# Performance work log

Hardware: AMD Instinct MI355X
Metric: run time of the kernel (lower is better)

The kernel has to match this reference:

```python
import jax, jax.numpy as jnp
import numpy as np

LR = 0.1          # learning_rate
THRESHOLD = 0.1   # surprise_threshold (fixed; adaptive_threshold=False / eval path)
TEMP = 0.1        # temperature
EPS = 1e-6

B, S, DK, DV = 64, 1024, 128, 128


def setup_inputs() -> dict:
    key = jax.random.key(0)
    k1, k2 = jax.random.split(key)
    return {
        "memory": jnp.zeros((B, DV, DK), dtype=jnp.float32),
        "key": jax.random.normal(k1, (B, S, DK), dtype=jnp.float32),
        "value": jax.random.normal(k2, (B, S, DV), dtype=jnp.float32),
    }


def reference(memory, key, value):
    # memory: (B, DV, DK); key: (B, S, DK); value: (B, S, DV)
    # Sequential delta-rule fast-weight update with surprise gating.
    def step(mem, kv):
        k_t, v_t = kv                                  # (B, DK), (B, DV)
        k_n = k_t / (jnp.linalg.norm(k_t, axis=-1, keepdims=True) + EPS)
        predicted = jnp.einsum('bvk,bk->bv', mem, k_n)  # (B, DV)
        surprise = predicted - v_t                      # (B, DV)
        s_norm = jnp.linalg.norm(surprise, axis=-1, keepdims=True)  # (B, 1)
        gate = jax.nn.sigmoid((s_norm - THRESHOLD) / TEMP)          # (B, 1)
        # forget_term + lr*learn_term = (predicted + lr*surprise) outer k_n
        update = (predicted + LR * surprise)[:, :, None] * k_n[:, None, :]
        mem = mem - gate[:, :, None] * update
        return mem, gate

    # scan over the sequence axis
    kv_seq = (jnp.swapaxes(key, 0, 1), jnp.swapaxes(value, 0, 1))  # (S, B, *)
    mem_final, gates = jax.lax.scan(step, memory, kv_seq)
    gate_values = jnp.swapaxes(gates, 0, 1)  # (B, S, 1)
    return mem_final, gate_values
```

## Files before the change

### kernel.cpp

```cpp
#include <hip/hip_runtime.h>
#include <math.h>

#define B_    64
#define S_    1024
#define DK_   128
#define DV_   128
#define T_    16
#define NC_   (S_ / T_)
#define KP_   (DK_ + 4)
#define LR_   0.1f
#define LRP1_ 1.1f
#define THR_  0.1f
#define ITEMP_ 10.0f
#define EPS_  1e-6f

template<int CTRL>
__device__ __forceinline__ float dpp_add(float x) {
  int t = __builtin_amdgcn_update_dpp(0, __float_as_int(x), CTRL, 0xf, 0xf, true);
  return x + __int_as_float(t);
}
__device__ __forceinline__ float wave_sum64(float x) {
  x = dpp_add<0x111>(x); x = dpp_add<0x112>(x); x = dpp_add<0x114>(x);
  x = dpp_add<0x118>(x); x = dpp_add<0x142>(x); x = dpp_add<0x143>(x);
  return __int_as_float(__builtin_amdgcn_readlane(__float_as_int(x), 63));
}
__device__ __forceinline__ float row16_sum(float x) {
  x = dpp_add<0x111>(x); x = dpp_add<0x112>(x);
  x = dpp_add<0x114>(x); x = dpp_add<0x118>(x);
  return x;
}
__device__ __forceinline__ float rdlane(float v, int l) {
  return __int_as_float(__builtin_amdgcn_readlane(__float_as_int(v), l));
}
__device__ __forceinline__ float dot4(float4 a, float4 b) {
  return fmaf(a.x, b.x, fmaf(a.y, b.y, fmaf(a.z, b.z, a.w * b.w)));
}
__device__ __forceinline__ void gll16(const float* g, float* l) {
  __builtin_amdgcn_global_load_lds(
      (const __attribute__((address_space(1))) unsigned int*)g,
      (__attribute__((address_space(3))) unsigned int*)l, 16, 0, 0);
}

__global__ __launch_bounds__(512, 1)
void sgm_kernel(const float* __restrict__ mem_in,
                const float* __restrict__ key,
                const float* __restrict__ value,
                float* __restrict__ out) {
  const int b = blockIdx.x, tid = threadIdx.x;
  const int g = tid >> 4, h = tid & 15, lane = tid & 63, wv = tid >> 6;

  __shared__ __align__(16) float kS[4][T_][KP_];
  __shared__ __align__(16) float vS[3][T_][KP_];
  __shared__ __align__(16) float rawL[T_][DK_];
  __shared__ __align__(16) float cuL[T_][DK_];
  __shared__ __align__(16) float GT[2][T_][T_];
  __shared__ __align__(16) float gateL[S_];

  float4 mA[4], mB[4];
  {
    const float4* Mp = reinterpret_cast<const float4*>(mem_in + (size_t)b * DV_ * DK_);
    #pragma unroll
    for (int rr = 0; rr < 4; ++rr) {
      mA[rr] = Mp[(4*g + rr) * 32 + h];
      mB[rr] = Mp[(4*g + rr) * 32 + 16 + h];
    }
  }
  const float* kb = key   + (size_t)b * S_ * DK_;
  const float* vb = value + (size_t)b * S_ * DV_;

  const int pPair = (tid - 64) >> 1;
  int tP = 0, jP = 0;
  {
    int t = 0, pp = pPair;
    if (wv > 0 && pPair >= 0 && pPair < 136) {
      while (pp > t) { pp -= (t + 1); ++t; }
      tP = t; jP = pp;
    }
  }

  auto stage = [&](int cc) {
    if (wv == 0 && lane < 32) {
      #pragma unroll
      for (int t = 0; t < T_; ++t)
        gll16(kb + (size_t)(cc*T_ + t)*DK_ + lane*4, &kS[cc & 3][t][0]);
    }
    if (wv == 1 && lane < 32) {
      #pragma unroll
      for (int t = 0; t < T_; ++t)
        gll16(vb + (size_t)(cc*T_ + t)*DV_ + lane*4, &vS[cc % 3][t][0]);
    }
  };

  float4 kxR[16];

  auto applyUpdate = [&](int sl) {
    #pragma unroll
    for (int j = 0; j < T_; ++j) {
      const float4* kj = reinterpret_cast<const float4*>(&kS[sl][j][0]);
      const float4 ky = kj[16 + h];
      const float4 cu = *reinterpret_cast<const float4*>(&cuL[j][4 * g]);
      const float cc4[4] = {cu.x, cu.y, cu.z, cu.w};
      #pragma unroll
      for (int rr = 0; rr < 4; ++rr) {
        mA[rr].x = fmaf(-cc4[rr], kxR[j].x, mA[rr].x);
        mA[rr].y = fmaf(-cc4[rr], kxR[j].y, mA[rr].y);
        mA[rr].z = fmaf(-cc4[rr], kxR[j].z, mA[rr].z);
        mA[rr].w = fmaf(-cc4[rr], kxR[j].w, mA[rr].w);
        mB[rr].x = fmaf(-cc4[rr], ky.x, mB[rr].x);
        mB[rr].y = fmaf(-cc4[rr], ky.y, mB[rr].y);
        mB[rr].z = fmaf(-cc4[rr], ky.z, mB[rr].z);
        mB[rr].w = fmaf(-cc4[rr], ky.w, mB[rr].w);
      }
    }
  };

  auto gramPhase = [&](int cc) {
    const int sl = cc & 3, pb = cc & 1;
    const int h2 = tid & 1;
    if (wv > 0 && pPair < 136) {
      const float4* kj4 = reinterpret_cast<const float4*>(&kS[sl][jP][h2*64]);
      const float4* kt4 = reinterpret_cast<const float4*>(&kS[sl][tP][h2*64]);
      float acc = 0.f;
      #pragma unroll
      for (int i = 0; i < 16; ++i) {
        const int ii = (i + pPair) & 15;
        acc += dot4(kj4[ii], kt4[ii]);
      }
      int sw = __builtin_amdgcn_update_dpp(0, __float_as_int(acc), 0xB1, 0xf, 0xf, true);
      const float tot = acc + __int_as_float(sw);
      if (h2 == 0) GT[pb][tP][jP] = tot;
    }
  };

  stage(0); stage(1);
  if (wv < 2) asm volatile("s_waitcnt vmcnt(0)" ::: "memory");
  __syncthreads();
  gramPhase(0);
  asm volatile("s_waitcnt lgkmcnt(0)" ::: "memory");
  __builtin_amdgcn_s_barrier();
  asm volatile("" ::: "memory");

  for (int c = 0; c < NC_; ++c) {
    const int cb = c & 1;
    const bool staged = (c + 2 < NC_);

    if (staged) stage(c + 2);

    if (c > 0) applyUpdate((c - 1) & 3);

    #pragma unroll
    for (int t = 0; t < T_; ++t) {
      const float4* kt = reinterpret_cast<const float4*>(&kS[c & 3][t][0]);
      const float4 kx = kt[h];
      const float4 ky = kt[16 + h];
      kxR[t] = kx;
      float a0 = dot4(mA[0], kx) + dot4(mB[0], ky);
      float a1 = dot4(mA[1], kx) + dot4(mB[1], ky);
      float a2 = dot4(mA[2], kx) + dot4(mB[2], ky);
      float a3 = dot4(mA[3], kx) + dot4(mB[3], ky);
      a0 = row16_sum(a0); a1 = row16_sum(a1);
      a2 = row16_sum(a2); a3 = row16_sum(a3);
      if (h == 15)
        *reinterpret_cast<float4*>(&rawL[t][4 * g]) = make_float4(a0, a1, a2, a3);
    }

    if (wv < 2) {
      if (staged) asm volatile("s_waitcnt vmcnt(16)" ::: "memory");
      else        asm volatile("s_waitcnt vmcnt(0)"  ::: "memory");
    }
    asm volatile("s_waitcnt lgkmcnt(0)" ::: "memory");
    __builtin_amdgcn_s_barrier();
    asm volatile("" ::: "memory");

    if (wv == 0) {
      const int sj = lane & 15;
      const float rinv = 1.0f / (sqrtf(GT[cb][sj][sj]) + EPS_);
      float cu0[T_], cu1[T_];
      #pragma unroll
      for (int t = 0; t < T_; ++t) {
        const float grt = GT[cb][t][sj];
        const float rin_t = rdlane(rinv, t);
        float y0 = 0.f, y1 = 0.f;
        #pragma unroll
        for (int j = 0; j < T_; ++j) if (j < t) {
          const float gjt = rdlane(grt, j);
          y0 = fmaf(gjt, cu0[j], y0);
          y1 = fmaf(gjt, cu1[j], y1);
        }
        const float2 rv  = *reinterpret_cast<const float2*>(&rawL[t][2*lane]);
        const float2 vvt = *reinterpret_cast<const float2*>(&vS[c % 3][t][2*lane]);
        const float pred0 = rin_t * (rv.x - y0);
        const float pred1 = rin_t * (rv.y - y1);
        const float s0 = pred0 - vvt.x, s1 = pred1 - vvt.y;
        const float s2 = wave_sum64(fmaf(s0, s0, s1 * s1));
        const float gg = 1.0f / (1.0f + __expf((THR_ - sqrtf(s2)) * ITEMP_));
        if (lane == 0) gateL[c*T_ + t] = gg;
        const float ct = gg * rin_t;
        const float u0 = fmaf(LRP1_, pred0, -(LR_ * vvt.x));
        const float u1 = fmaf(LRP1_, pred1, -(LR_ * vvt.y));
        cu0[t] = ct * u0; cu1[t] = ct * u1;
        *reinterpret_cast<float2*>(&cuL[t][2*lane]) = make_float2(cu0[t], cu1[t]);
      }
    } else {
      if (c + 1 < NC_) gramPhase(c + 1);
    }

    asm volatile("s_waitcnt lgkmcnt(0)" ::: "memory");
    __builtin_amdgcn_s_barrier();
    asm volatile("" ::: "memory");
  }

  applyUpdate((NC_ - 1) & 3);

  {
    float4* Op = reinterpret_cast<float4*>(out + (size_t)b * DV_ * DK_);
    #pragma unroll
    for (int rr = 0; rr < 4; ++rr) {
      Op[(4*g + rr) * 32 + h] = mA[rr];
      Op[(4*g + rr) * 32 + 16 + h] = mB[rr];
    }
    float2* Gp = reinterpret_cast<float2*>(out + (size_t)B_ * DV_ * DK_ + (size_t)b * S_);
    Gp[tid] = reinterpret_cast<const float2*>(gateL)[tid];
  }
}

extern "C" void kernel_launch(void* const* d_in, const int* in_sizes, int n_in,
                              void* d_out, int out_size, void* d_ws, size_t ws_size,
                              hipStream_t stream) {
  const float* mem = (const float*)d_in[0];
  const float* key = (const float*)d_in[1];
  const float* val = (const float*)d_in[2];
  float* out = (float*)d_out;
  sgm_kernel<<<B_, 512, 0, stream>>>(mem, key, val, out);
}
```

Measured before the change: 543.2 us.

## Add dedicated solver wave and pipeline chunk solve behind memory matvec

Adds a ninth wavefront that runs the sequential intra-chunk triangular solve and gating for chunk c-1, while the eight memory-holding waves compute raw predictions for chunk c. This lags the memory update by two chunks and corrects the raw predictions with a cross-chunk key Gram matrix (XG). The goal is one barrier per chunk instead of two, taking the serial wave-0 solve off the critical path. In exchange it adds a 16x16 cross-Gram computation per chunk, more LDS buffering, and reloads kx from LDS instead of keeping it in registers.

Result: slower. 790.8 us (+45.6%).

```diff
diff --git a/kernel.cpp b/kernel.cpp
--- a/kernel.cpp
+++ b/kernel.cpp
@@ -41,23 +41,26 @@
       (__attribute__((address_space(3))) unsigned int*)l, 16, 0, 0);
 }
 
-__global__ __launch_bounds__(512, 1)
+__global__ __launch_bounds__(576, 1)
 void sgm_kernel(const float* __restrict__ mem_in,
                 const float* __restrict__ key,
                 const float* __restrict__ value,
                 float* __restrict__ out) {
   const int b = blockIdx.x, tid = threadIdx.x;
-  const int g = tid >> 4, h = tid & 15, lane = tid & 63, wv = tid >> 6;
-
-  __shared__ __align__(16) float kS[4][T_][KP_];
-  __shared__ __align__(16) float vS[3][T_][KP_];
-  __shared__ __align__(16) float rawL[T_][DK_];
-  __shared__ __align__(16) float cuL[T_][DK_];
+  const int wv = tid >> 6;
+  const bool mW = (wv < 8);
+  const int g = tid >> 4, h = tid & 15, lane = tid & 63;
+
+  __shared__ __align__(16) float kS[5][T_][KP_];
+  __shared__ __align__(16) float vS[4][T_][KP_];
+  __shared__ __align__(16) float rawR[2][T_][DK_];
+  __shared__ __align__(16) float cuL[2][T_][DK_];
+  __shared__ __align__(16) float XG[2][T_][T_];
   __shared__ __align__(16) float GT[2][T_][T_];
   __shared__ __align__(16) float gateL[S_];
 
   float4 mA[4], mB[4];
-  {
+  if (mW) {
     const float4* Mp = reinterpret_cast<const float4*>(mem_in + (size_t)b * DV_ * DK_);
     #pragma unroll
     for (int rr = 0; rr < 4; ++rr) {
@@ -70,42 +73,41 @@
 
   const int pPair = (tid - 64) >> 1;
   int tP = 0, jP = 0;
-  {
+  if (mW && wv > 0 && pPair < 136) {
     int t = 0, pp = pPair;
-    if (wv > 0 && pPair >= 0 && pPair < 136) {
-      while (pp > t) { pp -= (t + 1); ++t; }
-      tP = t; jP = pp;
-    }
-  }
+    while (pp > t) { pp -= (t + 1); ++t; }
+    tP = t; jP = pp;
+  }
+  const int xId = tid - 64;
+  const int xj = (xId >> 4) & 15, xt = xId & 15;
 
   auto stage = [&](int cc) {
     if (wv == 0 && lane < 32) {
       #pragma unroll
       for (int t = 0; t < T_; ++t)
-        gll16(kb + (size_t)(cc*T_ + t)*DK_ + lane*4, &kS[cc & 3][t][0]);
+        gll16(kb + (size_t)(cc*T_ + t)*DK_ + lane*4, &kS[cc % 5][t][0]);
     }
     if (wv == 1 && lane < 32) {
       #pragma unroll
       for (int t = 0; t < T_; ++t)
-        gll16(vb + (size_t)(cc*T_ + t)*DV_ + lane*4, &vS[cc % 3][t][0]);
+        gll16(vb + (size_t)(cc*T_ + t)*DV_ + lane*4, &vS[cc & 3][t][0]);
     }
   };
 
-  float4 kxR[16];
-
-  auto applyUpdate = [&](int sl) {
+  auto applyUpdate = [&](int c2) {
+    const int sl = c2 % 5;
     #pragma unroll
     for (int j = 0; j < T_; ++j) {
       const float4* kj = reinterpret_cast<const float4*>(&kS[sl][j][0]);
-      const float4 ky = kj[16 + h];
-      const float4 cu = *reinterpret_cast<const float4*>(&cuL[j][4 * g]);
+      const float4 kx = kj[h], ky = kj[16 + h];
+      const float4 cu = *reinterpret_cast<const float4*>(&cuL[c2 & 1][j][4 * g]);
       const float cc4[4] = {cu.x, cu.y, cu.z, cu.w};
       #pragma unroll
       for (int rr = 0; rr < 4; ++rr) {
-        mA[rr].x = fmaf(-cc4[rr], kxR[j].x, mA[rr].x);
-        mA[rr].y = fmaf(-cc4[rr], kxR[j].y, mA[rr].y);
-        mA[rr].z = fmaf(-cc4[rr], kxR[j].z, mA[rr].z);
-        mA[rr].w = fmaf(-cc4[rr], kxR[j].w, mA[rr].w);
+        mA[rr].x = fmaf(-cc4[rr], kx.x, mA[rr].x);
+        mA[rr].y = fmaf(-cc4[rr], kx.y, mA[rr].y);
+        mA[rr].z = fmaf(-cc4[rr], kx.z, mA[rr].z);
+        mA[rr].w = fmaf(-cc4[rr], kx.w, mA[rr].w);
         mB[rr].x = fmaf(-cc4[rr], ky.x, mB[rr].x);
         mB[rr].y = fmaf(-cc4[rr], ky.y, mB[rr].y);
         mB[rr].z = fmaf(-cc4[rr], ky.z, mB[rr].z);
@@ -114,111 +116,139 @@
     }
   };
 
-  auto gramPhase = [&](int cc) {
-    const int sl = cc & 3, pb = cc & 1;
-    const int h2 = tid & 1;
-    if (wv > 0 && pPair < 136) {
-      const float4* kj4 = reinterpret_cast<const float4*>(&kS[sl][jP][h2*64]);
-      const float4* kt4 = reinterpret_cast<const float4*>(&kS[sl][tP][h2*64]);
-      float acc = 0.f;
-      #pragma unroll
-      for (int i = 0; i < 16; ++i) {
-        const int ii = (i + pPair) & 15;
-        acc += dot4(kj4[ii], kt4[ii]);
-      }
-      int sw = __builtin_amdgcn_update_dpp(0, __float_as_int(acc), 0xB1, 0xf, 0xf, true);
-      const float tot = acc + __int_as_float(sw);
-      if (h2 == 0) GT[pb][tP][jP] = tot;
-    }
-  };
-
   stage(0); stage(1);
   if (wv < 2) asm volatile("s_waitcnt vmcnt(0)" ::: "memory");
   __syncthreads();
-  gramPhase(0);
-  asm volatile("s_waitcnt lgkmcnt(0)" ::: "memory");
-  __builtin_amdgcn_s_barrier();
-  asm volatile("" ::: "memory");
-
-  for (int c = 0; c < NC_; ++c) {
+
+  for (int c = 0; c <= NC_; ++c) {
     const int cb = c & 1;
-    const bool staged = (c + 2 < NC_);
-
-    if (staged) stage(c + 2);
-
-    if (c > 0) applyUpdate((c - 1) & 3);
-
-    #pragma unroll
-    for (int t = 0; t < T_; ++t) {
-      const float4* kt = reinterpret_cast<const float4*>(&kS[c & 3][t][0]);
-      const float4 kx = kt[h];
-      const float4 ky = kt[16 + h];
-      kxR[t] = kx;
-      float a0 = dot4(mA[0], kx) + dot4(mB[0], ky);
-      float a1 = dot4(mA[1], kx) + dot4(mB[1], ky);
-      float a2 = dot4(mA[2], kx) + dot4(mB[2], ky);
-      float a3 = dot4(mA[3], kx) + dot4(mB[3], ky);
-      a0 = row16_sum(a0); a1 = row16_sum(a1);
-      a2 = row16_sum(a2); a3 = row16_sum(a3);
-      if (h == 15)
-        *reinterpret_cast<float4*>(&rawL[t][4 * g]) = make_float4(a0, a1, a2, a3);
+
+    if (mW) {
+      if (c < NC_) {
+        if (c + 2 < NC_) stage(c + 2);
+        if (c >= 2) applyUpdate(c - 2);
+
+        const int sl = c % 5;
+        #pragma unroll
+        for (int t = 0; t < T_; ++t) {
+          const float4* kt = reinterpret_cast<const float4*>(&kS[sl][t][0]);
+          const float4 kx = kt[h], ky = kt[16 + h];
+          float a0 = dot4(mA[0], kx) + dot4(mB[0], ky);
+          float a1 = dot4(mA[1], kx) + dot4(mB[1], ky);
+          float a2 = dot4(mA[2], kx) + dot4(mB[2], ky);
+          float a3 = dot4(mA[3], kx) + dot4(mB[3], ky);
+          a0 = row16_sum(a0); a1 = row16_sum(a1);
+          a2 = row16_sum(a2); a3 = row16_sum(a3);
+          if (h == 15)
+            *reinterpret_cast<float4*>(&rawR[cb][t][4 * g]) = make_float4(a0, a1, a2, a3);
+        }
+
+        if (c >= 1 && xId >= 0 && xId < 256) {
+          const float4* a4 = reinterpret_cast<const float4*>(&kS[(c - 1) % 5][xj][0]);
+          const float4* b4 = reinterpret_cast<const float4*>(&kS[sl][xt][0]);
+          float acc = 0.f;
+          #pragma unroll
+          for (int i = 0; i < 32; ++i) {
+            const int ii = (i + xId) & 31;
+            acc += dot4(a4[ii], b4[ii]);
+          }
+          XG[cb][xj][xt] = acc;
+        }
+
+        if (wv > 0 && pPair < 136) {
+          const int h2 = tid & 1;
+          const float4* kj4 = reinterpret_cast<const float4*>(&kS[sl][jP][h2 * 64]);
+          const float4* kt4 = reinterpret_cast<const float4*>(&kS[sl][tP][h2 * 64]);
+          float acc = 0.f;
+          #pragma unroll
+          for (int i = 0; i < 16; ++i) acc += dot4(kj4[i], kt4[i]);
+          int sw = __builtin_amdgcn_update_dpp(0, __float_as_int(acc), 0xB1, 0xf, 0xf, true);
+          const float tot = acc + __int_as_float(sw);
+          if (h2 == 0) GT[cb][tP][jP] = tot;
+        }
+      } else {
+        applyUpdate(NC_ - 2);
+      }
+    } else {
+      if (c >= 1) {
+        const int sc = c - 1, sb = sc & 1;
+        const int sl16 = lane & 15;
+
+        float rv0[T_], rv1[T_];
+        #pragma unroll
+        for (int t = 0; t < T_; ++t) {
+          const float2 rr = *reinterpret_cast<const float2*>(&rawR[sb][t][2 * lane]);
+          rv0[t] = rr.x; rv1[t] = rr.y;
+        }
+        if (sc >= 1) {
+          #pragma unroll
+          for (int j = 0; j < T_; ++j) {
+            const float2 cu2 = *reinterpret_cast<const float2*>(&cuL[(sc - 1) & 1][j][2 * lane]);
+            const float4* xr = reinterpret_cast<const float4*>(&XG[sb][j][0]);
+            const float4 x0 = xr[0], x1 = xr[1], x2 = xr[2], x3 = xr[3];
+            const float xv[16] = {x0.x,x0.y,x0.z,x0.w, x1.x,x1.y,x1.z,x1.w,
+                                  x2.x,x2.y,x2.z,x2.w, x3.x,x3.y,x3.z,x3.w};
+            #pragma unroll
+            for (int t = 0; t < T_; ++t) {
+              rv0[t] = fmaf(-cu2.x, xv[t], rv0[t]);
+              rv1[t] = fmaf(-cu2.y, xv[t], rv1[t]);
+            }
+          }
+        }
+
+        float Gr[T_];
+        #pragma unroll
+        for (int t = 0; t < T_; ++t) Gr[t] = GT[sb][t][sl16];
+        const float rinv = 1.0f / (sqrtf(GT[sb][sl16][sl16]) + EPS_);
+
+        float cu0[T_], cu1[T_];
+        #pragma unroll
+        for (int t = 0; t < T_; ++t) {
+          const float rin_t = rdlane(rinv, t);
+          float y0 = 0.f, y1 = 0.f;
+          #pragma unroll
+          for (int j = 0; j < T_; ++j) if (j < t) {
+            const float gjt = rdlane(Gr[t], j);
+            y0 = fmaf(gjt, cu0[j], y0);
+            y1 = fmaf(gjt, cu1[j], y1);
+          }
+          const float2 vvt = *reinterpret_cast<const float2*>(&vS[sc & 3][t][2 * lane]);
+          const float pred0 = rin_t * (rv0[t] - y0);
+          const float pred1 = rin_t * (rv1[t] - y1);
+          const float s0 = pred0 - vvt.x, s1 = pred1 - vvt.y;
+          const float s2 = wave_sum64(fmaf(s0, s0, s1 * s1));
+          const float gg = 1.0f / (1.0f + __expf((THR_ - sqrtf(s2)) * ITEMP_));
+          if (lane == 0) gateL[sc * T_ + t] = gg;
+          const float ct = gg * rin_t;
+          const float u0 = fmaf(LRP1_, pred0, -(LR_ * vvt.x));
+          const float u1 = fmaf(LRP1_, pred1, -(LR_ * vvt.y));
+          cu0[t] = ct * u0; cu1[t] = ct * u1;
+          *reinterpret_cast<float2*>(&cuL[sb][t][2 * lane]) = make_float2(cu0[t], cu1[t]);
+        }
+      }
     }
 
     if (wv < 2) {
-      if (staged) asm volatile("s_waitcnt vmcnt(16)" ::: "memory");
-      else        asm volatile("s_waitcnt vmcnt(0)"  ::: "memory");
+      if (c + 2 < NC_) asm volatile("s_waitcnt vmcnt(16)" ::: "memory");
+      else             asm volatile("s_waitcnt vmcnt(0)"  ::: "memory");
     }
     asm volatile("s_waitcnt lgkmcnt(0)" ::: "memory");
     __builtin_amdgcn_s_barrier();
     asm volatile("" ::: "memory");
-
-    if (wv == 0) {
-      const int sj = lane & 15;
-      const float rinv = 1.0f / (sqrtf(GT[cb][sj][sj]) + EPS_);
-      float cu0[T_], cu1[T_];
-      #pragma unroll
-      for (int t = 0; t < T_; ++t) {
-        const float grt = GT[cb][t][sj];
-        const float rin_t = rdlane(rinv, t);
-        float y0 = 0.f, y1 = 0.f;
-        #pragma unroll
-        for (int j = 0; j < T_; ++j) if (j < t) {
-          const float gjt = rdlane(grt, j);
-          y0 = fmaf(gjt, cu0[j], y0);
-          y1 = fmaf(gjt, cu1[j], y1);
-        }
-        const float2 rv  = *reinterpret_cast<const float2*>(&rawL[t][2*lane]);
-        const float2 vvt = *reinterpret_cast<const float2*>(&vS[c % 3][t][2*lane]);
-        const float pred0 = rin_t * (rv.x - y0);
-        const float pred1 = rin_t * (rv.y - y1);
-        const float s0 = pred0 - vvt.x, s1 = pred1 - vvt.y;
-        const float s2 = wave_sum64(fmaf(s0, s0, s1 * s1));
-        const float gg = 1.0f / (1.0f + __expf((THR_ - sqrtf(s2)) * ITEMP_));
-        if (lane == 0) gateL[c*T_ + t] = gg;
-        const float ct = gg * rin_t;
-        const float u0 = fmaf(LRP1_, pred0, -(LR_ * vvt.x));
-        const float u1 = fmaf(LRP1_, pred1, -(LR_ * vvt.y));
-        cu0[t] = ct * u0; cu1[t] = ct * u1;
-        *reinterpret_cast<float2*>(&cuL[t][2*lane]) = make_float2(cu0[t], cu1[t]);
-      }
-    } else {
-      if (c + 1 < NC_) gramPhase(c + 1);
-    }
-
-    asm volatile("s_waitcnt lgkmcnt(0)" ::: "memory");
-    __builtin_amdgcn_s_barrier();
-    asm volatile("" ::: "memory");
-  }
-
-  applyUpdate((NC_ - 1) & 3);
-
-  {
+  }
+
+  if (mW) applyUpdate(NC_ - 1);
+  __syncthreads();
+
+  if (mW) {
     float4* Op = reinterpret_cast<float4*>(out + (size_t)b * DV_ * DK_);
     #pragma unroll
     for (int rr = 0; rr < 4; ++rr) {
       Op[(4*g + rr) * 32 + h] = mA[rr];
       Op[(4*g + rr) * 32 + 16 + h] = mB[rr];
     }
+  }
+  if (tid < 512) {
     float2* Gp = reinterpret_cast<float2*>(out + (size_t)B_ * DV_ * DK_ + (size_t)b * S_);
     Gp[tid] = reinterpret_cast<const float2*>(gateL)[tid];
   }
@@ -231,5 +261,5 @@
   const float* key = (const float*)d_in[1];
   const float* val = (const float*)d_in[2];
   float* out = (float*)d_out;
-  sgm_kernel<<<B_, 512, 0, stream>>>(mem, key, val, out);
-}
+  sgm_kernel<<<B_, 576, 0, stream>>>(mem, key, val, out);
+}
```
